# Kernel optimization log

Measured on AMD Instinct MI355X. Metric: run time of the kernel, lower is better.

## Reference

```python
import jax, jax.numpy as jnp
import numpy as np

L = 2048          # instances (patches) per MIL bag
D_MODEL = 512
D_INNER = 512     # expand = 1
N_STATE = 128
DT_RANK = 32      # ceil(512 / 16)
K_CONV = 4
N_CLASSES = 2


def _mamba(u, in_w, conv_w, conv_b, xproj_w, dt_w, dt_b, A_log, Dp, out_w):
    """Canonical Mamba selective-scan block. u: [B, T, d_in]."""
    B, T, _ = u.shape
    xz = u @ in_w                                   # [B,T,2*D_INNER]
    x, z = jnp.split(xz, 2, axis=-1)                # [B,T,D_INNER] each
    # causal depthwise conv1d, kernel K_CONV
    xp = jnp.pad(x, ((0, 0), (K_CONV - 1, 0), (0, 0)))
    xc = conv_b
    for k in range(K_CONV):
        xc = xc + xp[:, k:k + T, :] * conv_w[:, k]
    x = jax.nn.silu(xc)
    x_dbl = x @ xproj_w                             # [B,T,R+2N]
    dt, Bm, Cm = jnp.split(x_dbl, [DT_RANK, DT_RANK + N_STATE], axis=-1)
    dt = jax.nn.softplus(dt @ dt_w + dt_b)          # [B,T,D_INNER]
    A = -jnp.exp(A_log)                             # [D_INNER,N]

    def step(h, inp):
        dt_t, B_t, C_t, x_t = inp                   # [B,D],[B,N],[B,N],[B,D]
        dA = jnp.exp(dt_t[:, :, None] * A)          # [B,D,N]
        h = h * dA + (dt_t * x_t)[:, :, None] * B_t[:, None, :]
        y = jnp.einsum('bdn,bn->bd', h, C_t)
        return h, y

    h0 = jnp.zeros((B, D_INNER, N_STATE), u.dtype)
    xs = (dt.transpose(1, 0, 2), Bm.transpose(1, 0, 2),
          Cm.transpose(1, 0, 2), x.transpose(1, 0, 2))
    _, ys = jax.lax.scan(jax.checkpoint(step), h0, xs)
    y = ys.transpose(1, 0, 2) + x * Dp
    y = y * jax.nn.silu(z)
    return y @ out_w


def setup_inputs() -> dict:
    key = jax.random.key(0)
    ks = jax.random.split(key, 8)
    nrm = lambda k, s, sc: jax.random.normal(k, s, jnp.float32) * sc

    def mamba_params(k, d_in):
        kk = jax.random.split(k, 6)
        return [
            nrm(kk[0], (d_in, 2 * D_INNER), d_in ** -0.5),                       # in_w
            nrm(kk[1], (D_INNER, K_CONV), 0.5),                                  # conv_w
            jnp.zeros((D_INNER,), jnp.float32),                                  # conv_b
            nrm(kk[2], (D_INNER, DT_RANK + 2 * N_STATE), D_INNER ** -0.5),       # xproj_w
            nrm(kk[3], (DT_RANK, D_INNER), DT_RANK ** -0.5),                     # dt_w
            jnp.full((D_INNER,), -4.6, jnp.float32) + nrm(kk[4], (D_INNER,), 0.1),  # dt_b
            jnp.log(jnp.tile(jnp.arange(1, N_STATE + 1, dtype=jnp.float32), (D_INNER, 1))),  # A_log
            jnp.ones((D_INNER,), jnp.float32),                                   # D
            nrm(kk[5], (D_INNER, D_MODEL), D_INNER ** -0.5),                     # out_w
        ]

    m = mamba_params(ks[0], D_MODEL)
    c = mamba_params(ks[1], 2 * D_MODEL)
    inp = {
        'x': nrm(ks[2], (1, L, 1024), 1.0),
        'feat_w': nrm(ks[3], (1024, D_MODEL), 1024 ** -0.5),
        'feat_b': jnp.zeros((D_MODEL,), jnp.float32),
        'cls1': nrm(ks[4], (1, 1, 1024), 1.0),
        'cls2': nrm(ks[5], (1, 1, 1024), 1.0),
        'cls_w': nrm(ks[6], (1024, N_CLASSES), 1024 ** -0.5),
        'cls_b': jnp.zeros((N_CLASSES,), jnp.float32),
    }
    names = ['in_w', 'conv_w', 'conv_b', 'xproj_w', 'dt_w', 'dt_b', 'A_log', 'D', 'out_w']
    for n, v in zip(names, m):
        inp['m_' + n] = v
    for n, v in zip(names, c):
        inp['c_' + n] = v
    return inp


def reference(x, feat_w, feat_b, cls1, cls2,
              m_in_w, m_conv_w, m_conv_b, m_xproj_w, m_dt_w, m_dt_b, m_A_log, m_D, m_out_w,
              c_in_w, c_conv_w, c_conv_b, c_xproj_w, c_dt_w, c_dt_b, c_A_log, c_D, c_out_w,
              cls_w, cls_b):
    f = jax.nn.relu(x @ feat_w + feat_b)            # [1,L,512]
    fi = jnp.flip(f, axis=1)
    mp = (m_in_w, m_conv_w, m_conv_b, m_xproj_w, m_dt_w, m_dt_b, m_A_log, m_D, m_out_w)
    cp = (c_in_w, c_conv_w, c_conv_b, c_xproj_w, c_dt_w, c_dt_b, c_A_log, c_D, c_out_w)
    yf = jax.nn.softmax(_mamba(f, *mp), axis=-1)    # simple_ssm shared for both dirs
    yi = jnp.flip(jax.nn.softmax(_mamba(fi, *mp), axis=-1), axis=1)
    seq_fi = jnp.concatenate([jnp.concatenate([yf, yi], axis=2), cls1], axis=1)  # [1,L+1,1024]
    seq_if = jnp.concatenate([jnp.concatenate([yi, yf], axis=2), cls2], axis=1)
    of = _mamba(seq_fi, *cp)                        # cross_ssm shared for both
    oi = _mamba(seq_if, *cp)
    cls = jnp.concatenate([of[:, -1, :], oi[:, -1, :]], axis=-1).squeeze()  # [1024]
    return (cls @ cls_w + cls_b)[None, :]           # [1, n_classes]
```

## Files before the change

### kernel.cpp

```cpp
#include <hip/hip_runtime.h>
#include <hip/hip_bf16.h>

#define TC    2049
#define DI    512
#define NS    128
#define XPN   288

typedef short bfx8 __attribute__((ext_vector_type(8)));
typedef float f32x4 __attribute__((ext_vector_type(4)));
typedef float f32x2 __attribute__((ext_vector_type(2)));

__device__ __forceinline__ float us2f(unsigned short u) {
    union { unsigned int i; float f; } v; v.i = ((unsigned int)u) << 16; return v.f;
}
__device__ __forceinline__ unsigned short f2bf(float f) {
    unsigned int u = __float_as_uint(f);
    u = (u + 0x7FFF + ((u >> 16) & 1)) >> 16;
    return (unsigned short)u;
}
__device__ __forceinline__ float sigm(float x) { return 1.f / (1.f + __expf(-x)); }

#define L2E 1.4426950408889634f

__device__ __forceinline__ float fexp2(float x) {
#if __has_builtin(__builtin_amdgcn_exp2f)
    return __builtin_amdgcn_exp2f(x);
#else
    return __expf(x * 0.6931471805599453f);
#endif
}

__global__ void detect_kernel(const unsigned short* __restrict__ x, int* __restrict__ flag) {
    __shared__ int cnt;
    int tid = threadIdx.x;
    if (tid == 0) cnt = 0;
    __syncthreads();
    unsigned short u = x[tid];
    int e = (u >> 7) & 0xFF;
    int insane = (u != 0 && (e < 97 || e > 157)) ? 1 : 0;
    atomicAdd(&cnt, insane);
    __syncthreads();
    if (tid == 0) *flag = (cnt >= 64) ? 1 : 0;
}

struct WD { const void* src; float* dst; int n; };
struct WDT { WD e[19]; };
__global__ __launch_bounds__(256) void widen_all_kernel(WDT tab, const int* __restrict__ flag) {
    WD d = tab.e[blockIdx.y];
    const int f = *flag;
    const int stride = gridDim.x * 256;
    int i = blockIdx.x * 256 + threadIdx.x;
    if (f) {
        const float* s = (const float*)d.src;
        for (; i < d.n; i += stride) d.dst[i] = s[i];
    } else {
        const unsigned short* s = (const unsigned short*)d.src;
        for (; i < d.n; i += stride) d.dst[i] = us2f(s[i]);
    }
}

__global__ __launch_bounds__(256) void wt_plain_kernel(
    const void* __restrict__ src, unsigned short* __restrict__ dst,
    int K, int N, const int* __restrict__ flag)
{
    int i = blockIdx.x * 256 + threadIdx.x;
    if (i >= K * N) return;
    int n = i / K, k = i - n * K;
    size_t si = (size_t)k * N + n;
    if (*flag) dst[i] = f2bf(((const float*)src)[si]);
    else       dst[i] = ((const unsigned short*)src)[si];
}

__global__ __launch_bounds__(256) void wt_xproj_kernel(
    const void* __restrict__ src, unsigned short* __restrict__ dst,
    const int* __restrict__ flag)
{
    int i = blockIdx.x * 256 + threadIdx.x;
    if (i >= 147456) return;
    int c = i >> 9, k = i & 511;
    int s;
    if (c < 32) s = c;
    else if (c < 160) { int q = c - 32;  s = 32  + (q >> 3) + ((q & 7) << 4); }
    else             { int q = c - 160; s = 160 + (q >> 3) + ((q & 7) << 4); }
    size_t si = (size_t)k * 288 + s;
    if (*flag) dst[i] = f2bf(((const float*)src)[si]);
    else       dst[i] = ((const unsigned short*)src)[si];
}

__global__ __launch_bounds__(256) void gemm_mfma_kernel(
    const float* __restrict__ A, int lda, long long sA,
    const unsigned short* __restrict__ Wt, int N, int K,
    const float* __restrict__ bias,
    float* __restrict__ C, int ldc, long long sC,
    int M, int act)
{
    A += (size_t)blockIdx.z * sA;
    C += (size_t)blockIdx.z * sC;
    __shared__ __align__(16) unsigned short As[64][40];
    __shared__ __align__(16) unsigned short Bs[64][40];
    const int tid = threadIdx.x;
    const int wave = tid >> 6, lane = tid & 63;
    const int bm = blockIdx.x * 64, bn = blockIdx.y * 64;
    const int col = lane & 15, quad = lane >> 4;

    f32x4 acc[4] = {{0.f,0.f,0.f,0.f},{0.f,0.f,0.f,0.f},{0.f,0.f,0.f,0.f},{0.f,0.f,0.f,0.f}};

    const int ar = tid >> 2, ak = (tid & 3) << 3;
    const int wn = tid & 63, wk = (tid >> 6) << 3;
    const bool wok = (bn + wn) < N;
    const unsigned short* wrow = Wt + (size_t)(bn + wn) * K;

    for (int kt = 0; kt < K; kt += 32) {
        float va[8];
        int gm = bm + ar;
        if (gm < M) {
            const float* ap = A + (size_t)gm * lda + kt + ak;
            float4 v0 = *(const float4*)ap;
            float4 v1 = *(const float4*)(ap + 4);
            va[0]=v0.x; va[1]=v0.y; va[2]=v0.z; va[3]=v0.w;
            va[4]=v1.x; va[5]=v1.y; va[6]=v1.z; va[7]=v1.w;
        } else {
#pragma unroll
            for (int j = 0; j < 8; ++j) va[j] = 0.f;
        }
        bfx8 bpk = {0,0,0,0,0,0,0,0};
        if (wok) bpk = *(const bfx8*)(wrow + kt + wk);
        __syncthreads();
        bfx8 apk;
#pragma unroll
        for (int j = 0; j < 8; ++j) apk[j] = (short)f2bf(va[j]);
        *(bfx8*)&As[ar][ak] = apk;
        *(bfx8*)&Bs[wn][wk] = bpk;
        __syncthreads();
        bfx8 af = *(const bfx8*)&As[wave * 16 + col][quad << 3];
#pragma unroll
        for (int ct = 0; ct < 4; ++ct) {
            bfx8 bf = *(const bfx8*)&Bs[ct * 16 + col][quad << 3];
            acc[ct] = __builtin_amdgcn_mfma_f32_16x16x32_bf16(af, bf, acc[ct], 0, 0, 0);
        }
    }
#pragma unroll
    for (int ct = 0; ct < 4; ++ct) {
        int gn = bn + ct * 16 + col;
        if (gn >= N) continue;
        float bv = bias ? bias[gn] : 0.f;
#pragma unroll
        for (int r = 0; r < 4; ++r) {
            int gm = bm + wave * 16 + quad * 4 + r;
            if (gm < M) {
                float v = acc[ct][r] + bv;
                if (act == 1) v = fmaxf(v, 0.f);
                C[(size_t)gm * ldc + gn] = v;
            }
        }
    }
}

__global__ __launch_bounds__(256) void conv_silu_kernel(
    const float* __restrict__ xzbase, int ld, long long bstride,
    const float* __restrict__ conv_w, const float* __restrict__ conv_b,
    float* __restrict__ xs, int T, int rev_mode)
{
    int idx = blockIdx.x * 256 + threadIdx.x;
    if (idx >= 2 * T * DI) return;
    int half = idx / (T * DI);
    int rem = idx - half * T * DI;
    int t = rem >> 9, d = rem & 511;
    const float* xzp = xzbase + (rev_mode ? 0 : (size_t)half * bstride);
    int rev = rev_mode ? half : 0;
    float acc = conv_b[d];
#pragma unroll
    for (int k = 0; k < 4; ++k) {
        int tt = t - 3 + k;
        if (tt >= 0) {
            int g = rev ? (T - 1 - tt) : tt;
            acc += conv_w[d * 4 + k] * xzp[(size_t)g * ld + d];
        }
    }
    xs[idx] = acc * sigm(acc);
}

__global__ __launch_bounds__(256) void dt_kernel(
    const float* __restrict__ xdbl, const float* __restrict__ dt_w,
    const float* __restrict__ dt_b, float* __restrict__ dtout, int T)
{
    int idx = blockIdx.x * 256 + threadIdx.x;
    if (idx >= 2 * T * DI) return;
    int half = idx / (T * DI);
    int rem = idx - half * T * DI;
    int t = rem >> 9, j = rem & 511;
    const float* a = xdbl + (size_t)half * T * XPN + (size_t)t * XPN;
    float acc = dt_b[j];
#pragma unroll
    for (int k = 0; k < 32; ++k) acc += a[k] * dt_w[k * DI + j];
    dtout[idx] = (acc > 20.f) ? acc : log1pf(__expf(acc));
}

__global__ __launch_bounds__(256) void silu_z_kernel(float* __restrict__ xz, int n)
{
    int idx = blockIdx.x * 256 + threadIdx.x;
    if (idx >= n) return;
    int t = idx >> 9, d = idx & 511;
    float* p = xz + (size_t)t * 1024 + 512 + d;
    float z = *p;
    *p = z * sigm(z);
}

__global__ __launch_bounds__(256) void scan_part1_kernel(
    const float* __restrict__ dt, const float* __restrict__ xdbl,
    const float* __restrict__ xs, const float* __restrict__ A_log,
    float* __restrict__ Sarr, float* __restrict__ H, int T, int NC, int LC)
{
    int b = blockIdx.x * 4 + (threadIdx.x >> 6);
    int c = b % NC;
    int dp = b / NC;
    int hd0 = dp * 4;
    int half = hd0 >> 9;
    int lane = threadIdx.x & 63;
    int sub = lane >> 4, l = lane & 15;
    int hd = hd0 + sub;
    int d = hd & 511;
    f32x2 a2[4];
#pragma unroll
    for (int q = 0; q < 4; ++q) {
        a2[q][0] = -__expf(A_log[d * NS + 32 * q + l])      * L2E;
        a2[q][1] = -__expf(A_log[d * NS + 32 * q + 16 + l]) * L2E;
    }
    int t0 = c * LC, t1 = min(T, t0 + LC);
    const float* dtp = dt + (size_t)half * T * DI + (size_t)t0 * DI + d;
    const float* xsp = xs + (size_t)half * T * DI + (size_t)t0 * DI + d;
    const float* row = xdbl + (size_t)half * T * XPN + (size_t)t0 * XPN;
    const int bo = 32 + 8 * l;
    float S = 0.f;
    f32x2 h2[4] = {{0.f,0.f},{0.f,0.f},{0.f,0.f},{0.f,0.f}};
    int t = t0;
    for (; t + 2 <= t1; t += 2) {
        float dva = dtp[0],  xva = xsp[0];
        float dvb = dtp[DI], xvb = xsp[DI];
        float4 v0 = *(const float4*)(row + bo);
        float4 v1 = *(const float4*)(row + bo + 4);
        float4 w0 = *(const float4*)(row + XPN + bo);
        float4 w1 = *(const float4*)(row + XPN + bo + 4);
        f32x2 Ba[4] = {{v0.x,v0.y},{v0.z,v0.w},{v1.x,v1.y},{v1.z,v1.w}};
        f32x2 Bb[4] = {{w0.x,w0.y},{w0.z,w0.w},{w1.x,w1.y},{w1.z,w1.w}};
        float ua = dva * xva, ub = dvb * xvb;
        S += dva + dvb;
        f32x2 ua2 = {ua, ua}, ub2 = {ub, ub};
        f32x2 dva2 = {dva, dva}, dvb2 = {dvb, dvb};
#pragma unroll
        for (int q = 0; q < 4; ++q) {
            f32x2 ga = dva2 * a2[q];
            f32x2 ea; ea[0] = fexp2(ga[0]); ea[1] = fexp2(ga[1]);
            h2[q] = h2[q] * ea + ua2 * Ba[q];
            f32x2 gb = dvb2 * a2[q];
            f32x2 eb; eb[0] = fexp2(gb[0]); eb[1] = fexp2(gb[1]);
            h2[q] = h2[q] * eb + ub2 * Bb[q];
        }
        dtp += 2 * DI; xsp += 2 * DI; row += 2 * XPN;
    }
    for (; t < t1; ++t) {
        float dv = *dtp, xv = *xsp;
        float4 v0 = *(const float4*)(row + bo);
        float4 v1 = *(const float4*)(row + bo + 4);
        f32x2 Bv[4] = {{v0.x,v0.y},{v0.z,v0.w},{v1.x,v1.y},{v1.z,v1.w}};
        float u = dv * xv;
        S += dv;
        f32x2 u2 = {u, u}, dv2 = {dv, dv};
#pragma unroll
        for (int q = 0; q < 4; ++q) {
            f32x2 g = dv2 * a2[q];
            f32x2 e; e[0] = fexp2(g[0]); e[1] = fexp2(g[1]);
            h2[q] = h2[q] * e + u2 * Bv[q];
        }
        dtp += DI; xsp += DI; row += XPN;
    }
    size_t base = ((size_t)hd * NC + c) * 128 + l;
#pragma unroll
    for (int q = 0; q < 4; ++q) {
        H[base + 32 * q]      = h2[q][0];
        H[base + 32 * q + 16] = h2[q][1];
    }
    if (l == 0) Sarr[(size_t)hd * NC + c] = S;
}

__global__ __launch_bounds__(128) void scan_combine_kernel(
    const float* __restrict__ Sarr, float* __restrict__ H,
    const float* __restrict__ A_log, float* __restrict__ Hfinal, int NC)
{
    int hd = blockIdx.x;
    int d = hd & 511;
    int n = threadIdx.x;
    float a = -__expf(A_log[d * NS + n]) * L2E;
    size_t base = (size_t)hd * NC * 128 + n;
    float h = 0.f;
    for (int c = 0; c < NC; ++c) {
        size_t off = base + (size_t)c * 128;
        float p = fexp2(a * Sarr[(size_t)hd * NC + c]);
        float hh = H[off];
        H[off] = h;
        h = p * h + hh;
    }
    if (Hfinal) Hfinal[(size_t)hd * 128 + n] = h;
}

__global__ __launch_bounds__(256) void scan_emit_kernel(
    const float* __restrict__ dt, const float* __restrict__ xdbl,
    const float* __restrict__ xs, const float* __restrict__ xz,
    const float* __restrict__ A_log, const float* __restrict__ Hstart,
    const float* __restrict__ Dp,
    float* __restrict__ y, int T, int NC, int LC)
{
    int b = blockIdx.x * 4 + (threadIdx.x >> 6);
    int c = b % NC;
    int dp = b / NC;
    int hd0 = dp * 4;
    int half = hd0 >> 9;
    int lane = threadIdx.x & 63;
    int sub = lane >> 4, l = lane & 15;
    int hd = hd0 + sub;
    int d = hd & 511;
    f32x2 a2[4];
#pragma unroll
    for (int q = 0; q < 4; ++q) {
        a2[q][0] = -__expf(A_log[d * NS + 32 * q + l])      * L2E;
        a2[q][1] = -__expf(A_log[d * NS + 32 * q + 16 + l]) * L2E;
    }
    const float Dv = Dp[d];
    size_t base = ((size_t)hd * NC + c) * 128 + l;
    f32x2 h2[4];
#pragma unroll
    for (int q = 0; q < 4; ++q) {
        h2[q][0] = Hstart[base + 32 * q];
        h2[q][1] = Hstart[base + 32 * q + 16];
    }
    int t0 = c * LC, t1 = min(T, t0 + LC);
    size_t lin = (size_t)half * T * DI + (size_t)t0 * DI + d;
    const float* dtp = dt + lin;
    const float* xsp = xs + lin;
    float* yp = y + lin;
    const float* row = xdbl + (size_t)half * T * XPN + (size_t)t0 * XPN;
    const float* zp;
    long long zs;
    if (half == 0) { zp = xz + (size_t)t0 * 1024 + 512 + d;           zs = 1024;  }
    else           { zp = xz + (size_t)(T - 1 - t0) * 1024 + 512 + d; zs = -1024; }
    const int bo = 32 + 8 * l;
    const int co = 160 + 8 * l;
    int t = t0;
    for (; t + 2 <= t1; t += 2) {
        float dva = dtp[0],  xva = xsp[0];
        float dvb = dtp[DI], xvb = xsp[DI];
        float ga = zp[0], gb = zp[zs];
        float4 v0 = *(const float4*)(row + bo);
        float4 v1 = *(const float4*)(row + bo + 4);
        float4 c0 = *(const float4*)(row + co);
        float4 c1 = *(const float4*)(row + co + 4);
        float4 w0 = *(const float4*)(row + XPN + bo);
        float4 w1 = *(const float4*)(row + XPN + bo + 4);
        float4 e0 = *(const float4*)(row + XPN + co);
        float4 e1 = *(const float4*)(row + XPN + co + 4);
        f32x2 Ba[4] = {{v0.x,v0.y},{v0.z,v0.w},{v1.x,v1.y},{v1.z,v1.w}};
        f32x2 Ca[4] = {{c0.x,c0.y},{c0.z,c0.w},{c1.x,c1.y},{c1.z,c1.w}};
        f32x2 Bb[4] = {{w0.x,w0.y},{w0.z,w0.w},{w1.x,w1.y},{w1.z,w1.w}};
        f32x2 Cb[4] = {{e0.x,e0.y},{e0.z,e0.w},{e1.x,e1.y},{e1.z,e1.w}};
        float ua = dva * xva, ub = dvb * xvb;
        f32x2 ua2 = {ua, ua}, ub2 = {ub, ub};
        f32x2 dva2 = {dva, dva}, dvb2 = {dvb, dvb};
        f32x2 pa2 = {0.f, 0.f}, pb2 = {0.f, 0.f};
#pragma unroll
        for (int q = 0; q < 4; ++q) {
            f32x2 gaa = dva2 * a2[q];
            f32x2 ea; ea[0] = fexp2(gaa[0]); ea[1] = fexp2(gaa[1]);
            h2[q] = h2[q] * ea + ua2 * Ba[q];
            pa2 += h2[q] * Ca[q];
        }
#pragma unroll
        for (int q = 0; q < 4; ++q) {
            f32x2 gbb = dvb2 * a2[q];
            f32x2 eb; eb[0] = fexp2(gbb[0]); eb[1] = fexp2(gbb[1]);
            h2[q] = h2[q] * eb + ub2 * Bb[q];
            pb2 += h2[q] * Cb[q];
        }
        float pa = pa2[0] + pa2[1], pb = pb2[0] + pb2[1];
        pa += __shfl_xor(pa, 1, 64);  pb += __shfl_xor(pb, 1, 64);
        pa += __shfl_xor(pa, 2, 64);  pb += __shfl_xor(pb, 2, 64);
        pa += __shfl_xor(pa, 4, 64);  pb += __shfl_xor(pb, 4, 64);
        pa += __shfl_xor(pa, 8, 64);  pb += __shfl_xor(pb, 8, 64);
        if (l == 0) {
            yp[0]  = (pa + xva * Dv) * ga;
            yp[DI] = (pb + xvb * Dv) * gb;
        }
        dtp += 2 * DI; xsp += 2 * DI; row += 2 * XPN; yp += 2 * DI; zp += 2 * zs;
    }
    for (; t < t1; ++t) {
        float dv = *dtp, xv = *xsp;
        float gv = zp[0];
        float4 v0 = *(const float4*)(row + bo);
        float4 v1 = *(const float4*)(row + bo + 4);
        float4 c0 = *(const float4*)(row + co);
        float4 c1 = *(const float4*)(row + co + 4);
        f32x2 Bv[4] = {{v0.x,v0.y},{v0.z,v0.w},{v1.x,v1.y},{v1.z,v1.w}};
        f32x2 Cv[4] = {{c0.x,c0.y},{c0.z,c0.w},{c1.x,c1.y},{c1.z,c1.w}};
        float u = dv * xv;
        f32x2 u2 = {u, u}, dv2 = {dv, dv};
        f32x2 p2 = {0.f, 0.f};
#pragma unroll
        for (int q = 0; q < 4; ++q) {
            f32x2 g = dv2 * a2[q];
            f32x2 e; e[0] = fexp2(g[0]); e[1] = fexp2(g[1]);
            h2[q] = h2[q] * e + u2 * Bv[q];
            p2 += h2[q] * Cv[q];
        }
        float p = p2[0] + p2[1];
        p += __shfl_xor(p, 1, 64);
        p += __shfl_xor(p, 2, 64);
        p += __shfl_xor(p, 4, 64);
        p += __shfl_xor(p, 8, 64);
        if (l == 0) *yp = (p + xv * Dv) * gv;
        dtp += DI; xsp += DI; row += XPN; yp += DI; zp += zs;
    }
}

__global__ __launch_bounds__(64) void cross_readout_kernel(
    const float* __restrict__ Hfinal, const float* __restrict__ xdbl,
    const float* __restrict__ xs, const float* __restrict__ xz,
    const float* __restrict__ Dp, float* __restrict__ ylast, int T)
{
    int hd = blockIdx.x;
    int half = hd >> 9, d = hd & 511;
    int lane = threadIdx.x;
    xdbl += (size_t)half * T * XPN;
    xs   += (size_t)half * T * DI;
    xz   += (size_t)half * T * 1024;
    float h0 = Hfinal[(size_t)hd * 128 + lane];
    float h1 = Hfinal[(size_t)hd * 128 + 64 + lane];
    const float* xl = xdbl + (size_t)(T - 1) * XPN;
    int pos = 160 + (lane & 15) * 8 + (lane >> 4);
    float C0 = xl[pos];
    float C1 = xl[pos + 4];
    float p = h0 * C0 + h1 * C1;
#pragma unroll
    for (int off = 32; off > 0; off >>= 1) p += __shfl_down(p, off, 64);
    if (lane == 0) {
        float xlast = xs[(size_t)(T - 1) * DI + d];
        float zl = xz[(size_t)(T - 1) * 1024 + 512 + d];
        ylast[half * DI + d] = (p + xlast * Dp[d]) * (zl * sigm(zl));
    }
}

__global__ __launch_bounds__(256) void softmax_scatter_kernel(
    const float* __restrict__ yo, float* __restrict__ seq, int T)
{
    __shared__ float sm[4];
    const int t = blockIdx.x, half = blockIdx.y, tid = threadIdx.x;
    const float* row = yo + (size_t)half * T * DI + (size_t)t * DI;
    float v0 = row[tid], v1 = row[tid + 256];
    float m = fmaxf(v0, v1);
#pragma unroll
    for (int o = 32; o > 0; o >>= 1) m = fmaxf(m, __shfl_xor(m, o, 64));
    if ((tid & 63) == 0) sm[tid >> 6] = m;
    __syncthreads();
    m = fmaxf(fmaxf(sm[0], sm[1]), fmaxf(sm[2], sm[3]));
    __syncthreads();
    float e0 = __expf(v0 - m), e1 = __expf(v1 - m);
    float s = e0 + e1;
#pragma unroll
    for (int o = 32; o > 0; o >>= 1) s += __shfl_xor(s, o, 64);
    if ((tid & 63) == 0) sm[tid >> 6] = s;
    __syncthreads();
    s = sm[0] + sm[1] + sm[2] + sm[3];
    float inv = 1.f / s;
    e0 *= inv; e1 *= inv;
    float* seq_fi = seq;
    float* seq_if = seq + (size_t)TC * 1024;
    if (half == 0) {
        float* d1 = seq_fi + (size_t)t * 1024;
        float* d2 = seq_if + (size_t)t * 1024 + 512;
        d1[tid] = e0; d1[tid + 256] = e1;
        d2[tid] = e0; d2[tid + 256] = e1;
    } else {
        int tg = T - 1 - t;
        float* d1 = seq_fi + (size_t)tg * 1024 + 512;
        float* d2 = seq_if + (size_t)tg * 1024;
        d1[tid] = e0; d1[tid + 256] = e1;
        d2[tid] = e0; d2[tid + 256] = e1;
    }
}

__global__ __launch_bounds__(256) void cls_rows_kernel(
    const float* __restrict__ cls1, const float* __restrict__ cls2,
    float* __restrict__ seq)
{
    int i = blockIdx.x * 256 + threadIdx.x;
    if (i < 1024)
        seq[(size_t)(TC - 1) * 1024 + i] = cls1[i];
    else
        seq[(size_t)TC * 1024 + (size_t)(TC - 1) * 1024 + (i - 1024)] = cls2[i - 1024];
}

__global__ __launch_bounds__(256) void vecmat_kernel(
    const float* __restrict__ ylast, const float* __restrict__ Wout,
    float* __restrict__ olast)
{
    int half = blockIdx.y;
    int j = blockIdx.x * 256 + threadIdx.x;
    const float* v = ylast + half * DI;
    float acc = 0.f;
    for (int k = 0; k < DI; ++k) acc += v[k] * Wout[k * DI + j];
    olast[half * DI + j] = acc;
}

__global__ __launch_bounds__(256) void final_kernel(
    const float* __restrict__ ol, const float* __restrict__ cw,
    const float* __restrict__ cb, float* __restrict__ out)
{
    __shared__ float s0[4], s1[4];
    int tid = threadIdx.x;
    float a0 = 0.f, a1 = 0.f;
    for (int j = tid; j < 1024; j += 256) {
        float v = ol[j];
        a0 += v * cw[2 * j];
        a1 += v * cw[2 * j + 1];
    }
#pragma unroll
    for (int o = 32; o > 0; o >>= 1) { a0 += __shfl_xor(a0, o, 64); a1 += __shfl_xor(a1, o, 64); }
    if ((tid & 63) == 0) { s0[tid >> 6] = a0; s1[tid >> 6] = a1; }
    __syncthreads();
    if (tid == 0) {
        out[0] = s0[0] + s0[1] + s0[2] + s0[3] + cb[0];
        out[1] = s1[0] + s1[1] + s1[2] + s1[3] + cb[1];
    }
}

extern "C" void kernel_launch(void* const* d_in, const int* in_sizes, int n_in,
                              void* d_out, int out_size, void* d_ws, size_t ws_size,
                              hipStream_t stream)
{
    float* out = (float*)d_out;
    float* ws = (float*)d_ws;

    static const int sig_map[25] = {0,1,2,3,4,23,24,5,6,7,8,9,10,11,12,13,
                                    14,15,16,17,18,19,20,21,22};
    int idx[25];
    bool dict_order = (n_in >= 7 && in_sizes[6] == 2);
    for (int i = 0; i < 25; ++i) idx[i] = dict_order ? i : sig_map[i];

    const size_t A0 = 0;
    const size_t B0 = 2098176;
    const size_t C0 = 3278400;
    const size_t D0 = 5375552;
    const size_t E0 = 7472704;
    const size_t F0 = 8652352;
    const size_t G0 = 10749504;
    const size_t YL0 = 14945856;
    const size_t OL0 = 14946880;
    const size_t DT_S = A0;
    const size_t S_S  = B0;
    const size_t H_S  = G0;
    const size_t DT_C = 7474752;
    const size_t H_C  = 9572928;
    const size_t S_C  = 13898304;
    const size_t HFIN = 14029376;
    size_t o = 14947904;
    const size_t P_FEATW = o; o += 524288;
    const size_t P_FEATB = o; o += 512;
    const size_t P_CLS1  = o; o += 1024;
    const size_t P_CLS2  = o; o += 1024;
    const size_t P_CLSW  = o; o += 2048;
    const size_t P_CLSB  = o; o += 4;
    const size_t P_MINW  = o; o += 524288;
    const size_t P_MCW   = o; o += 2048;
    const size_t P_MCB   = o; o += 512;
    const size_t P_MXP   = o; o += 147456;
    const size_t P_MDTW  = o; o += 16384;
    const size_t P_MDTB  = o; o += 512;
    const size_t P_MAL   = o; o += 65536;
    const size_t P_MD    = o; o += 512;
    const size_t P_MOW   = o; o += 262144;
    const size_t P_CINW  = o; o += 1048576;
    const size_t P_CCW   = o; o += 2048;
    const size_t P_CCB   = o; o += 512;
    const size_t P_CXP   = o; o += 147456;
    const size_t P_CDTW  = o; o += 16384;
    const size_t P_CDTB  = o; o += 512;
    const size_t P_CAL   = o; o += 65536;
    const size_t P_CD    = o; o += 512;
    const size_t P_COW   = o; o += 262144;
    const size_t OFF_FLAG = o;

    int* flagp = (int*)(ws + OFF_FLAG);
    unsigned short* WT_FEATW = (unsigned short*)(ws + P_FEATW);
    unsigned short* WT_MINW  = (unsigned short*)(ws + P_MINW);
    unsigned short* WT_MXP   = (unsigned short*)(ws + P_MXP);
    unsigned short* WT_MOW   = (unsigned short*)(ws + P_MOW);
    unsigned short* WT_CINW  = (unsigned short*)(ws + P_CINW);
    unsigned short* WT_CXP   = (unsigned short*)(ws + P_CXP);

    detect_kernel<<<1, 256, 0, stream>>>((const unsigned short*)d_in[idx[0]], flagp);

    WDT tab;
    const int lg[19]  = {0,2,3,4,5,6,8,9,11,12,13,14,17,18,20,21,22,23,24};
    const int nsl[25] = {2097152, 524288, 512, 1024, 1024, 2048, 2,
                         524288, 2048, 512, 147456, 16384, 512, 65536, 512, 262144,
                         1048576, 2048, 512, 147456, 16384, 512, 65536, 512, 262144};
    float* dstl[25] = {
        ws + A0, nullptr, ws + P_FEATB, ws + P_CLS1, ws + P_CLS2,
        ws + P_CLSW, ws + P_CLSB,
        nullptr, ws + P_MCW, ws + P_MCB, nullptr, ws + P_MDTW, ws + P_MDTB,
        ws + P_MAL, ws + P_MD, nullptr,
        nullptr, ws + P_CCW, ws + P_CCB, nullptr, ws + P_CDTW, ws + P_CDTB,
        ws + P_CAL, ws + P_CD, ws + P_COW};
    for (int i = 0; i < 19; ++i) {
        int s = lg[i];
        tab.e[i].src = d_in[idx[s]];
        tab.e[i].dst = dstl[s];
        tab.e[i].n = nsl[s];
    }
    widen_all_kernel<<<dim3(128, 19), 256, 0, stream>>>(tab, flagp);
    wt_plain_kernel<<<2048, 256, 0, stream>>>(d_in[idx[1]],  WT_FEATW, 1024, 512,  flagp);
    wt_plain_kernel<<<2048, 256, 0, stream>>>(d_in[idx[7]],  WT_MINW,  512,  1024, flagp);
    wt_plain_kernel<<<1024, 256, 0, stream>>>(d_in[idx[15]], WT_MOW,   512,  512,  flagp);
    wt_plain_kernel<<<4096, 256, 0, stream>>>(d_in[idx[16]], WT_CINW,  1024, 1024, flagp);
    wt_xproj_kernel<<<576, 256, 0, stream>>>(d_in[idx[10]], WT_MXP, flagp);
    wt_xproj_kernel<<<576, 256, 0, stream>>>(d_in[idx[19]], WT_CXP, flagp);

    gemm_mfma_kernel<<<dim3(32, 8, 1), 256, 0, stream>>>(ws + A0, 1024, 0, WT_FEATW, 512, 1024,
                                                         ws + P_FEATB, ws + B0, 512, 0,
                                                         2048, 1);
    gemm_mfma_kernel<<<dim3(32, 16, 1), 256, 0, stream>>>(ws + B0, 512, 0, WT_MINW, 1024, 512,
                                                          nullptr, ws + C0, 1024, 0,
                                                          2048, 0);
    conv_silu_kernel<<<8192, 256, 0, stream>>>(ws + C0, 1024, 0, ws + P_MCW, ws + P_MCB,
                                               ws + D0, 2048, 1);
    silu_z_kernel<<<4096, 256, 0, stream>>>(ws + C0, 2048 * DI);
    gemm_mfma_kernel<<<dim3(32, 5, 2), 256, 0, stream>>>(ws + D0, 512, 2048LL * 512, WT_MXP,
                                                         288, 512, nullptr, ws + E0, 288,
                                                         2048LL * 288, 2048, 0);
    dt_kernel<<<8192, 256, 0, stream>>>(ws + E0, ws + P_MDTW, ws + P_MDTB, ws + DT_S, 2048);
    scan_part1_kernel<<<2048, 256, 0, stream>>>(ws + DT_S, ws + E0, ws + D0, ws + P_MAL,
                                                ws + S_S, ws + H_S, 2048, 32, 64);
    scan_combine_kernel<<<1024, 128, 0, stream>>>(ws + S_S, ws + H_S, ws + P_MAL, nullptr, 32);
    scan_emit_kernel<<<2048, 256, 0, stream>>>(ws + DT_S, ws + E0, ws + D0, ws + C0,
                                               ws + P_MAL, ws + H_S, ws + P_MD,
                                               ws + F0, 2048, 32, 64);
    gemm_mfma_kernel<<<dim3(32, 8, 2), 256, 0, stream>>>(ws + F0, 512, 2048LL * 512, WT_MOW,
                                                         512, 512, nullptr, ws + A0, 512,
                                                         2048LL * 512, 2048, 0);
    cls_rows_kernel<<<8, 256, 0, stream>>>(ws + P_CLS1, ws + P_CLS2, ws + G0);
    softmax_scatter_kernel<<<dim3(2048, 2), 256, 0, stream>>>(ws + A0, ws + G0, 2048);
    gemm_mfma_kernel<<<dim3(33, 16, 2), 256, 0, stream>>>(ws + G0, 1024, 2049LL * 1024, WT_CINW,
                                                          1024, 1024, nullptr, ws + C0, 1024,
                                                          2049LL * 1024, 2049, 0);
    conv_silu_kernel<<<8196, 256, 0, stream>>>(ws + C0, 1024, 2049LL * 1024, ws + P_CCW,
                                               ws + P_CCB, ws + A0, 2049, 0);
    gemm_mfma_kernel<<<dim3(33, 5, 2), 256, 0, stream>>>(ws + A0, 512, 2049LL * 512, WT_CXP,
                                                         288, 512, nullptr, ws + B0, 288,
                                                         2049LL * 288, 2049, 0);
    dt_kernel<<<8196, 256, 0, stream>>>(ws + B0, ws + P_CDTW, ws + P_CDTB, ws + DT_C, 2049);
    scan_part1_kernel<<<2112, 256, 0, stream>>>(ws + DT_C, ws + B0, ws + A0, ws + P_CAL,
                                                ws + S_C, ws + H_C, 2049, 33, 64);
    scan_combine_kernel<<<1024, 128, 0, stream>>>(ws + S_C, ws + H_C, ws + P_CAL, ws + HFIN, 33);
    cross_readout_kernel<<<1024, 64, 0, stream>>>(ws + HFIN, ws + B0, ws + A0, ws + C0,
                                                  ws + P_CD, ws + YL0, 2049);
    vecmat_kernel<<<dim3(2, 2), 256, 0, stream>>>(ws + YL0, ws + P_COW, ws + OL0);
    final_kernel<<<1, 256, 0, stream>>>(ws + OL0, ws + P_CLSW, ws + P_CLSB, out);
}
```

Baseline: 597.9 us.

## Store GEMM A-operands as bf16 in producers instead of fp32 buffers

Several intermediate activations (the input x, the feature output, the scan output y and the softmaxed sequence) are now written directly as bf16 by their producer kernels. The GEMM kernel gains flags to read A as bf16 and write C as bf16. This halves the memory traffic for these buffers and drops the per-tile fp32-to-bf16 conversion inside the GEMM. The workspace layout is adjusted so the bf16 buffers do not overlap the scan scratch. Rounding now happens at the producer, but the GEMM already rounded these same values to bf16 before, so the numerics should be nearly unchanged.

```diff
diff --git a/kernel.cpp b/kernel.cpp
--- a/kernel.cpp
+++ b/kernel.cpp
@@ -44,7 +44,7 @@
 }
 
 struct WD { const void* src; float* dst; int n; };
-struct WDT { WD e[19]; };
+struct WDT { WD e[18]; };
 __global__ __launch_bounds__(256) void widen_all_kernel(WDT tab, const int* __restrict__ flag) {
     WD d = tab.e[blockIdx.y];
     const int f = *flag;
@@ -59,6 +59,15 @@
     }
 }
 
+__global__ __launch_bounds__(256) void x2bf_kernel(
+    const void* __restrict__ src, unsigned short* __restrict__ dst, int n,
+    const int* __restrict__ flag)
+{
+    int i = blockIdx.x * 256 + threadIdx.x;
+    if (i >= n) return;
+    dst[i] = (*flag) ? f2bf(((const float*)src)[i]) : ((const unsigned short*)src)[i];
+}
+
 __global__ __launch_bounds__(256) void wt_plain_kernel(
     const void* __restrict__ src, unsigned short* __restrict__ dst,
     int K, int N, const int* __restrict__ flag)
@@ -88,14 +97,12 @@
 }
 
 __global__ __launch_bounds__(256) void gemm_mfma_kernel(
-    const float* __restrict__ A, int lda, long long sA,
+    const void* __restrict__ Ain, int lda, long long sA,
     const unsigned short* __restrict__ Wt, int N, int K,
     const float* __restrict__ bias,
-    float* __restrict__ C, int ldc, long long sC,
-    int M, int act)
-{
-    A += (size_t)blockIdx.z * sA;
-    C += (size_t)blockIdx.z * sC;
+    void* __restrict__ Cout, int ldc, long long sC,
+    int M, int act, int a_bf16, int c_bf16)
+{
     __shared__ __align__(16) unsigned short As[64][40];
     __shared__ __align__(16) unsigned short Bs[64][40];
     const int tid = threadIdx.x;
@@ -109,26 +116,29 @@
     const int wn = tid & 63, wk = (tid >> 6) << 3;
     const bool wok = (bn + wn) < N;
     const unsigned short* wrow = Wt + (size_t)(bn + wn) * K;
+    const int gm = bm + ar;
+    const unsigned short* abf = (const unsigned short*)Ain + (size_t)blockIdx.z * sA
+                                + (size_t)gm * lda;
+    const float* af32 = (const float*)Ain + (size_t)blockIdx.z * sA + (size_t)gm * lda;
 
     for (int kt = 0; kt < K; kt += 32) {
-        float va[8];
-        int gm = bm + ar;
+        bfx8 apk = {0,0,0,0,0,0,0,0};
         if (gm < M) {
-            const float* ap = A + (size_t)gm * lda + kt + ak;
-            float4 v0 = *(const float4*)ap;
-            float4 v1 = *(const float4*)(ap + 4);
-            va[0]=v0.x; va[1]=v0.y; va[2]=v0.z; va[3]=v0.w;
-            va[4]=v1.x; va[5]=v1.y; va[6]=v1.z; va[7]=v1.w;
-        } else {
-#pragma unroll
-            for (int j = 0; j < 8; ++j) va[j] = 0.f;
+            if (a_bf16) {
+                apk = *(const bfx8*)(abf + kt + ak);
+            } else {
+                const float* ap = af32 + kt + ak;
+                float4 v0 = *(const float4*)ap;
+                float4 v1 = *(const float4*)(ap + 4);
+                apk[0]=(short)f2bf(v0.x); apk[1]=(short)f2bf(v0.y);
+                apk[2]=(short)f2bf(v0.z); apk[3]=(short)f2bf(v0.w);
+                apk[4]=(short)f2bf(v1.x); apk[5]=(short)f2bf(v1.y);
+                apk[6]=(short)f2bf(v1.z); apk[7]=(short)f2bf(v1.w);
+            }
         }
         bfx8 bpk = {0,0,0,0,0,0,0,0};
         if (wok) bpk = *(const bfx8*)(wrow + kt + wk);
         __syncthreads();
-        bfx8 apk;
-#pragma unroll
-        for (int j = 0; j < 8; ++j) apk[j] = (short)f2bf(va[j]);
         *(bfx8*)&As[ar][ak] = apk;
         *(bfx8*)&Bs[wn][wk] = bpk;
         __syncthreads();
@@ -146,11 +156,13 @@
         float bv = bias ? bias[gn] : 0.f;
 #pragma unroll
         for (int r = 0; r < 4; ++r) {
-            int gm = bm + wave * 16 + quad * 4 + r;
-            if (gm < M) {
+            int gmo = bm + wave * 16 + quad * 4 + r;
+            if (gmo < M) {
                 float v = acc[ct][r] + bv;
                 if (act == 1) v = fmaxf(v, 0.f);
-                C[(size_t)gm * ldc + gn] = v;
+                size_t co = (size_t)blockIdx.z * sC + (size_t)gmo * ldc + gn;
+                if (c_bf16) ((unsigned short*)Cout)[co] = f2bf(v);
+                else        ((float*)Cout)[co] = v;
             }
         }
     }
@@ -308,7 +320,7 @@
     const float* __restrict__ xs, const float* __restrict__ xz,
     const float* __restrict__ A_log, const float* __restrict__ Hstart,
     const float* __restrict__ Dp,
-    float* __restrict__ y, int T, int NC, int LC)
+    unsigned short* __restrict__ y, int T, int NC, int LC)
 {
     int b = blockIdx.x * 4 + (threadIdx.x >> 6);
     int c = b % NC;
@@ -337,7 +349,7 @@
     size_t lin = (size_t)half * T * DI + (size_t)t0 * DI + d;
     const float* dtp = dt + lin;
     const float* xsp = xs + lin;
-    float* yp = y + lin;
+    unsigned short* yp = y + lin;
     const float* row = xdbl + (size_t)half * T * XPN + (size_t)t0 * XPN;
     const float* zp;
     long long zs;
@@ -386,8 +398,8 @@
         pa += __shfl_xor(pa, 4, 64);  pb += __shfl_xor(pb, 4, 64);
         pa += __shfl_xor(pa, 8, 64);  pb += __shfl_xor(pb, 8, 64);
         if (l == 0) {
-            yp[0]  = (pa + xva * Dv) * ga;
-            yp[DI] = (pb + xvb * Dv) * gb;
+            yp[0]  = f2bf((pa + xva * Dv) * ga);
+            yp[DI] = f2bf((pb + xvb * Dv) * gb);
         }
         dtp += 2 * DI; xsp += 2 * DI; row += 2 * XPN; yp += 2 * DI; zp += 2 * zs;
     }
@@ -415,7 +427,7 @@
         p += __shfl_xor(p, 2, 64);
         p += __shfl_xor(p, 4, 64);
         p += __shfl_xor(p, 8, 64);
-        if (l == 0) *yp = (p + xv * Dv) * gv;
+        if (l == 0) *yp = f2bf((p + xv * Dv) * gv);
         dtp += DI; xsp += DI; row += XPN; yp += DI; zp += zs;
     }
 }
@@ -448,7 +460,7 @@
 }
 
 __global__ __launch_bounds__(256) void softmax_scatter_kernel(
-    const float* __restrict__ yo, float* __restrict__ seq, int T)
+    const float* __restrict__ yo, unsigned short* __restrict__ seq, int T)
 {
     __shared__ float sm[4];
     const int t = blockIdx.x, half = blockIdx.y, tid = threadIdx.x;
@@ -469,32 +481,32 @@
     __syncthreads();
     s = sm[0] + sm[1] + sm[2] + sm[3];
     float inv = 1.f / s;
-    e0 *= inv; e1 *= inv;
-    float* seq_fi = seq;
-    float* seq_if = seq + (size_t)TC * 1024;
+    unsigned short b0 = f2bf(e0 * inv), b1 = f2bf(e1 * inv);
+    unsigned short* seq_fi = seq;
+    unsigned short* seq_if = seq + (size_t)TC * 1024;
     if (half == 0) {
-        float* d1 = seq_fi + (size_t)t * 1024;
-        float* d2 = seq_if + (size_t)t * 1024 + 512;
-        d1[tid] = e0; d1[tid + 256] = e1;
-        d2[tid] = e0; d2[tid + 256] = e1;
+        unsigned short* d1 = seq_fi + (size_t)t * 1024;
+        unsigned short* d2 = seq_if + (size_t)t * 1024 + 512;
+        d1[tid] = b0; d1[tid + 256] = b1;
+        d2[tid] = b0; d2[tid + 256] = b1;
     } else {
         int tg = T - 1 - t;
-        float* d1 = seq_fi + (size_t)tg * 1024 + 512;
-        float* d2 = seq_if + (size_t)tg * 1024;
-        d1[tid] = e0; d1[tid + 256] = e1;
-        d2[tid] = e0; d2[tid + 256] = e1;
+        unsigned short* d1 = seq_fi + (size_t)tg * 1024 + 512;
+        unsigned short* d2 = seq_if + (size_t)tg * 1024;
+        d1[tid] = b0; d1[tid + 256] = b1;
+        d2[tid] = b0; d2[tid + 256] = b1;
     }
 }
 
 __global__ __launch_bounds__(256) void cls_rows_kernel(
     const float* __restrict__ cls1, const float* __restrict__ cls2,
-    float* __restrict__ seq)
+    unsigned short* __restrict__ seq)
 {
     int i = blockIdx.x * 256 + threadIdx.x;
     if (i < 1024)
-        seq[(size_t)(TC - 1) * 1024 + i] = cls1[i];
+        seq[(size_t)(TC - 1) * 1024 + i] = f2bf(cls1[i]);
     else
-        seq[(size_t)TC * 1024 + (size_t)(TC - 1) * 1024 + (i - 1024)] = cls2[i - 1024];
+        seq[(size_t)TC * 1024 + (size_t)(TC - 1) * 1024 + (i - 1024)] = f2bf(cls2[i - 1024]);
 }
 
 __global__ __launch_bounds__(256) void vecmat_kernel(
@@ -554,7 +566,7 @@
     const size_t YL0 = 14945856;
     const size_t OL0 = 14946880;
     const size_t DT_S = A0;
-    const size_t S_S  = B0;
+    const size_t S_S  = B0 + 524288;
     const size_t H_S  = G0;
     const size_t DT_C = 7474752;
     const size_t H_C  = 9572928;
@@ -588,6 +600,10 @@
     const size_t OFF_FLAG = o;
 
     int* flagp = (int*)(ws + OFF_FLAG);
+    unsigned short* XB   = (unsigned short*)(ws + A0);
+    unsigned short* FB   = (unsigned short*)(ws + B0);
+    unsigned short* YB   = (unsigned short*)(ws + F0);
+    unsigned short* SEQB = (unsigned short*)(ws + G0);
     unsigned short* WT_FEATW = (unsigned short*)(ws + P_FEATW);
     unsigned short* WT_MINW  = (unsigned short*)(ws + P_MINW);
     unsigned short* WT_MXP   = (unsigned short*)(ws + P_MXP);
@@ -598,24 +614,25 @@
     detect_kernel<<<1, 256, 0, stream>>>((const unsigned short*)d_in[idx[0]], flagp);
 
     WDT tab;
-    const int lg[19]  = {0,2,3,4,5,6,8,9,11,12,13,14,17,18,20,21,22,23,24};
+    const int lg[18]  = {2,3,4,5,6,8,9,11,12,13,14,17,18,20,21,22,23,24};
     const int nsl[25] = {2097152, 524288, 512, 1024, 1024, 2048, 2,
                          524288, 2048, 512, 147456, 16384, 512, 65536, 512, 262144,
                          1048576, 2048, 512, 147456, 16384, 512, 65536, 512, 262144};
     float* dstl[25] = {
-        ws + A0, nullptr, ws + P_FEATB, ws + P_CLS1, ws + P_CLS2,
+        nullptr, nullptr, ws + P_FEATB, ws + P_CLS1, ws + P_CLS2,
         ws + P_CLSW, ws + P_CLSB,
         nullptr, ws + P_MCW, ws + P_MCB, nullptr, ws + P_MDTW, ws + P_MDTB,
         ws + P_MAL, ws + P_MD, nullptr,
         nullptr, ws + P_CCW, ws + P_CCB, nullptr, ws + P_CDTW, ws + P_CDTB,
         ws + P_CAL, ws + P_CD, ws + P_COW};
-    for (int i = 0; i < 19; ++i) {
+    for (int i = 0; i < 18; ++i) {
         int s = lg[i];
         tab.e[i].src = d_in[idx[s]];
         tab.e[i].dst = dstl[s];
         tab.e[i].n = nsl[s];
     }
-    widen_all_kernel<<<dim3(128, 19), 256, 0, stream>>>(tab, flagp);
+    widen_all_kernel<<<dim3(128, 18), 256, 0, stream>>>(tab, flagp);
+    x2bf_kernel<<<8192, 256, 0, stream>>>(d_in[idx[0]], XB, 2097152, flagp);
     wt_plain_kernel<<<2048, 256, 0, stream>>>(d_in[idx[1]],  WT_FEATW, 1024, 512,  flagp);
     wt_plain_kernel<<<2048, 256, 0, stream>>>(d_in[idx[7]],  WT_MINW,  512,  1024, flagp);
     wt_plain_kernel<<<1024, 256, 0, stream>>>(d_in[idx[15]], WT_MOW,   512,  512,  flagp);
@@ -623,38 +640,38 @@
     wt_xproj_kernel<<<576, 256, 0, stream>>>(d_in[idx[10]], WT_MXP, flagp);
     wt_xproj_kernel<<<576, 256, 0, stream>>>(d_in[idx[19]], WT_CXP, flagp);
 
-    gemm_mfma_kernel<<<dim3(32, 8, 1), 256, 0, stream>>>(ws + A0, 1024, 0, WT_FEATW, 512, 1024,
-                                                         ws + P_FEATB, ws + B0, 512, 0,
-                                                         2048, 1);
-    gemm_mfma_kernel<<<dim3(32, 16, 1), 256, 0, stream>>>(ws + B0, 512, 0, WT_MINW, 1024, 512,
+    gemm_mfma_kernel<<<dim3(32, 8, 1), 256, 0, stream>>>(XB, 1024, 0, WT_FEATW, 512, 1024,
+                                                         ws + P_FEATB, FB, 512, 0,
+                                                         2048, 1, 1, 1);
+    gemm_mfma_kernel<<<dim3(32, 16, 1), 256, 0, stream>>>(FB, 512, 0, WT_MINW, 1024, 512,
                                                           nullptr, ws + C0, 1024, 0,
-                                                          2048, 0);
+                                                          2048, 0, 1, 0);
     conv_silu_kernel<<<8192, 256, 0, stream>>>(ws + C0, 1024, 0, ws + P_MCW, ws + P_MCB,
                                                ws + D0, 2048, 1);
     silu_z_kernel<<<4096, 256, 0, stream>>>(ws + C0, 2048 * DI);
     gemm_mfma_kernel<<<dim3(32, 5, 2), 256, 0, stream>>>(ws + D0, 512, 2048LL * 512, WT_MXP,
                                                          288, 512, nullptr, ws + E0, 288,
-                                                         2048LL * 288, 2048, 0);
+                                                         2048LL * 288, 2048, 0, 0, 0);
     dt_kernel<<<8192, 256, 0, stream>>>(ws + E0, ws + P_MDTW, ws + P_MDTB, ws + DT_S, 2048);
     scan_part1_kernel<<<2048, 256, 0, stream>>>(ws + DT_S, ws + E0, ws + D0, ws + P_MAL,
                                                 ws + S_S, ws + H_S, 2048, 32, 64);
     scan_combine_kernel<<<1024, 128, 0, stream>>>(ws + S_S, ws + H_S, ws + P_MAL, nullptr, 32);
     scan_emit_kernel<<<2048, 256, 0, stream>>>(ws + DT_S, ws + E0, ws + D0, ws + C0,
                                                ws + P_MAL, ws + H_S, ws + P_MD,
-                                               ws + F0, 2048, 32, 64);
-    gemm_mfma_kernel<<<dim3(32, 8, 2), 256, 0, stream>>>(ws + F0, 512, 2048LL * 512, WT_MOW,
+                                               YB, 2048, 32, 64);
+    gemm_mfma_kernel<<<dim3(32, 8, 2), 256, 0, stream>>>(YB, 512, 2048LL * 512, WT_MOW,
                                                          512, 512, nullptr, ws + A0, 512,
-                                                         2048LL * 512, 2048, 0);
-    cls_rows_kernel<<<8, 256, 0, stream>>>(ws + P_CLS1, ws + P_CLS2, ws + G0);
-    softmax_scatter_kernel<<<dim3(2048, 2), 256, 0, stream>>>(ws + A0, ws + G0, 2048);
-    gemm_mfma_kernel<<<dim3(33, 16, 2), 256, 0, stream>>>(ws + G0, 1024, 2049LL * 1024, WT_CINW,
+                                                         2048LL * 512, 2048, 0, 1, 0);
+    cls_rows_kernel<<<8, 256, 0, stream>>>(ws + P_CLS1, ws + P_CLS2, SEQB);
+    softmax_scatter_kernel<<<dim3(2048, 2), 256, 0, stream>>>(ws + A0, SEQB, 2048);
+    gemm_mfma_kernel<<<dim3(33, 16, 2), 256, 0, stream>>>(SEQB, 1024, 2049LL * 1024, WT_CINW,
                                                           1024, 1024, nullptr, ws + C0, 1024,
-                                                          2049LL * 1024, 2049, 0);
+                                                          2049LL * 1024, 2049, 0, 1, 0);
     conv_silu_kernel<<<8196, 256, 0, stream>>>(ws + C0, 1024, 2049LL * 1024, ws + P_CCW,
                                                ws + P_CCB, ws + A0, 2049, 0);
     gemm_mfma_kernel<<<dim3(33, 5, 2), 256, 0, stream>>>(ws + A0, 512, 2049LL * 512, WT_CXP,
                                                          288, 512, nullptr, ws + B0, 288,
-                                                         2049LL * 288, 2049, 0);
+                                                         2049LL * 288, 2049, 0, 0, 0);
     dt_kernel<<<8196, 256, 0, stream>>>(ws + B0, ws + P_CDTW, ws + P_CDTB, ws + DT_C, 2049);
     scan_part1_kernel<<<2112, 256, 0, stream>>>(ws + DT_C, ws + B0, ws + A0, ws + P_CAL,
                                                 ws + S_C, ws + H_C, 2049, 33, 64);
```

Result: faster. 571.8 us (-4.4%).
